# Optimization experiments

Measured on AMD Instinct MI355X. Metric: run time of the kernel, lower is better.

Reference implementation:

```python
import jax, jax.numpy as jnp
import numpy as np

B, C, H8, W8 = 2, 256, 56, 96
RADIUS, LEVELS = 4, 4


def setup_inputs() -> dict:
    key = jax.random.key(0)
    k1, k2, k3, k4, k5 = jax.random.split(key, 5)
    fmap1 = jax.random.normal(k1, (B, C, H8, W8), jnp.float32)
    fmap2 = jax.random.normal(k2, (B, C, H8, W8), jnp.float32)
    xs = jnp.arange(W8, dtype=jnp.float32)
    ys = jnp.arange(H8, dtype=jnp.float32)
    bx, by = jnp.broadcast_arrays(xs[None, :], ys[:, None])
    base = jnp.stack([bx, by], axis=0)  # [2,H8,W8], x first (as create_coords_grid)
    coords = base[None] + 4.0 * jax.random.normal(k3, (B, 2, H8, W8), jnp.float32)
    flow = jax.random.normal(k4, (B, 2, H8, W8), jnp.float32)
    mask = jax.random.normal(k5, (B, 9 * 8 * 8, H8, W8), jnp.float32)
    return {"fmap1": fmap1, "fmap2": fmap2, "coords": coords, "flow": flow, "mask": mask}


def _bilinear_sample(cflat, Hl, Wl, px, py):
    # cflat: [N, Hl*Wl]; px,py: [N,P] pixel coords; zero padding outside (grid_sample default)
    x0 = jnp.floor(px)
    y0 = jnp.floor(py)
    wx = px - x0
    wy = py - y0
    x0 = x0.astype(jnp.int32)
    y0 = y0.astype(jnp.int32)

    def g(xi, yi):
        valid = (xi >= 0) & (xi <= Wl - 1) & (yi >= 0) & (yi <= Hl - 1)
        idx = jnp.clip(yi, 0, Hl - 1) * Wl + jnp.clip(xi, 0, Wl - 1)
        return jnp.where(valid, jnp.take_along_axis(cflat, idx, axis=1), 0.0)

    return ((1 - wy) * ((1 - wx) * g(x0, y0) + wx * g(x0 + 1, y0))
            + wy * ((1 - wx) * g(x0, y0 + 1) + wx * g(x0 + 1, y0 + 1)))


def _corr_lookup(fmap1, fmap2, coords):
    b, c, h, w = fmap1.shape
    n = b * h * w
    # all-pairs correlation, scaled by sqrt(C)
    corr = jnp.einsum('bchw,bcij->bhwij', fmap1, fmap2) / jnp.sqrt(jnp.float32(c))
    cl = corr.reshape(n, h, w)
    # query coords (pixel units at level 0)
    cx = coords[:, 0].reshape(n)
    cy = coords[:, 1].reshape(n)
    r = RADIUS
    lin = jnp.linspace(-r, r, 2 * r + 1, dtype=jnp.float32)
    # replicates torch.meshgrid(dy,dx) quirk: x-offset varies along axis 0, y along axis 1
    xo = jnp.repeat(lin, 2 * r + 1)  # [81]
    yo = jnp.tile(lin, 2 * r + 1)    # [81]
    outs = []
    for i in range(LEVELS):
        Hl, Wl = cl.shape[1], cl.shape[2]
        cflat = cl.reshape(n, Hl * Wl)
        px = cx[:, None] / (2 ** i) + xo[None, :]
        py = cy[:, None] / (2 ** i) + yo[None, :]
        samp = _bilinear_sample(cflat, Hl, Wl, px, py)  # [N,81]
        outs.append(samp.reshape(b, h, w, -1))
        if i < LEVELS - 1:  # 2x2 avg pool, stride 2
            cl = cl.reshape(n, Hl // 2, 2, Wl // 2, 2).mean(axis=(2, 4))
    out = jnp.concatenate(outs, axis=-1)  # [B,h,w,4*81]
    return out.transpose(0, 3, 1, 2)


def _convex_upsample(flow, mask):
    b, ch, h, w = flow.shape
    m = mask.reshape(b, 1, 9, 8, 8, h, w)
    m = jax.nn.softmax(m, axis=2)
    fp = jnp.pad(8.0 * flow, ((0, 0), (0, 0), (1, 1), (1, 1)))
    # 3x3 unfold, kernel positions row-major (matches F.unfold ordering)
    patches = jnp.stack([fp[:, :, i:i + h, j:j + w]
                         for i in range(3) for j in range(3)], axis=2)  # [B,2,9,h,w]
    up = jnp.sum(m * patches[:, :, :, None, None], axis=2)  # [B,2,8,8,h,w]
    up = up.transpose(0, 1, 4, 2, 5, 3)  # [B,2,h,8,w,8]
    return up.reshape(b, ch, 8 * h, 8 * w)


def reference(fmap1, fmap2, coords, flow, mask):
    corr_feats = _corr_lookup(fmap1, fmap2, coords)  # [B,324,H8,W8]
    up_flow = _convex_upsample(flow, mask)           # [B,2,8*H8,8*W8]
    return (corr_feats, up_flow)
```

## Files before the change

### kernel.cpp

```cpp
#include <hip/hip_runtime.h>
#include <math.h>

constexpr int B = 2, C = 256, H = 56, W = 96;
constexpr int HW = H * W;
constexpr int RADIUS = 4;

#define SQ 21.166666f
constexpr float SCL = 36.0f / (127.0f * 127.0f * 16.0f);

constexpr size_t F1T_B = 0;
constexpr size_t L0_B  = (size_t)B * HW * C;
constexpr size_t L1_B  = L0_B + (size_t)B * HW * C;
constexpr size_t L2_B  = L1_B + (size_t)B * 28 * 48 * C;
constexpr size_t L3_B  = L2_B + (size_t)B * 14 * 24 * C;
constexpr size_t OUT0_ELEMS = (size_t)B * 324 * HW;

static __device__ __forceinline__ int dot4acc(int a, int b, int c) {
#if __has_builtin(__builtin_amdgcn_sdot4)
    return __builtin_amdgcn_sdot4(a, b, c, false);
#else
    c += (int)(char)(a) * (int)(char)(b);
    c += (int)(char)(a >> 8) * (int)(char)(b >> 8);
    c += (int)(char)(a >> 16) * (int)(char)(b >> 16);
    c += (int)(char)(a >> 24) * (int)(char)(b >> 24);
    return c;
#endif
}

static __device__ __forceinline__ unsigned short pack_i8x2(float a, float b) {
    int ia = (int)rintf(a); ia = ia < -127 ? -127 : (ia > 127 ? 127 : ia);
    int ib = (int)rintf(b); ib = ib < -127 ? -127 : (ib > 127 ? 127 : ib);
    return (unsigned short)((ia & 0xFF) | ((ib & 0xFF) << 8));
}

constexpr int TP_BLOCKS = (HW / 32) * (C / 64) * 2 * B;
constexpr int CU_BLOCKS = B * H * 8;
__global__ __launch_bounds__(256) void prep_kernel(
    const float* __restrict__ fmap1, const float* __restrict__ fmap2,
    const float* __restrict__ flow, const float* __restrict__ mask,
    char* __restrict__ ws, float* __restrict__ out1) {
    __shared__ float smem[72 * 96 + 2 * 3 * 98];
    int bid = blockIdx.x;
    int tid = threadIdx.x;

    if (bid < TP_BLOCKS) {
        float (*tile)[33] = (float(*)[33])smem;
        int zi = bid / 672;
        int rem = bid % 672;
        int by = rem / 168, bx = rem % 168;
        int b = zi & 1, m = zi >> 1;
        const float* src = m ? fmap2 : fmap1;
        unsigned short* dst = (unsigned short*)(ws + (m ? L0_B : F1T_B));
        int c0 = by * 64, q0 = bx * 32;
        int tx = tid & 31, ty = tid >> 5;
#pragma unroll
        for (int r = 0; r < 8; ++r) {
            int cl = ty + r * 8;
            tile[cl][tx] = src[((size_t)(b * C + c0 + cl)) * HW + q0 + tx];
        }
        __syncthreads();
#pragma unroll
        for (int r = 0; r < 4; ++r) {
            int pl = ty + r * 8;
            dst[((size_t)b * HW + q0 + pl) * 128 + (c0 >> 1) + tx] =
                pack_i8x2(tile[2 * tx][pl] * SQ, tile[2 * tx + 1][pl] * SQ);
        }
        return;
    }

    float* msk = smem;
    float* fst = smem + 72 * 96;
    int cb = bid - TP_BLOCKS;
    int i = cb & 7;
    int r = cb >> 3;
    int h = r % H;
    int b = r / H;

    for (int idx = tid; idx < 72 * 96; idx += 256) {
        int row = idx / 96, wc = idx - row * 96;
        int k = row >> 3, j = row & 7;
        int gl = k * 64 + i * 8 + j;
        msk[idx] = mask[((size_t)(b * 576 + gl)) * HW + h * W + wc];
    }
    for (int idx = tid; idx < 588; idx += 256) {
        int ch = idx / 294;
        int rem2 = idx - ch * 294;
        int rr = rem2 / 98;
        int xw = rem2 - rr * 98;
        int hh = h + rr - 1, ww = xw - 1;
        float v = 0.f;
        if (hh >= 0 && hh < H && ww >= 0 && ww < W)
            v = 8.0f * flow[((size_t)(b * 2 + ch)) * HW + hh * W + ww];
        fst[idx] = v;
    }
    __syncthreads();

#pragma unroll
    for (int rr = 0; rr < 3; ++rr) {
        int col = tid + rr * 256;
        int w = col >> 3, j = col & 7;
        float m[9], mx = -1e30f;
#pragma unroll
        for (int k = 0; k < 9; ++k) {
            m[k] = msk[(k * 8 + j) * 96 + w];
            mx = fmaxf(mx, m[k]);
        }
        float sum = 0.f;
#pragma unroll
        for (int k = 0; k < 9; ++k) {
            m[k] = __expf(m[k] - mx);
            sum += m[k];
        }
        float inv = 1.0f / sum;
        float a0 = 0.f, a1 = 0.f;
#pragma unroll
        for (int k = 0; k < 9; ++k) {
            int ki = k / 3, kj = k - ki * 3;
            float wgt = m[k] * inv;
            a0 = fmaf(wgt, fst[0 * 294 + ki * 98 + w + kj], a0);
            a1 = fmaf(wgt, fst[1 * 294 + ki * 98 + w + kj], a1);
        }
        size_t row8 = (size_t)8 * h + i;
        out1[((size_t)(b * 2 + 0) * 448 + row8) * 768 + col] = a0;
        out1[((size_t)(b * 2 + 1) * 448 + row8) * 768 + col] = a1;
    }
}

constexpr int NP1 = B * 28 * 48 * C / 2;
constexpr int NP2 = B * 14 * 24 * C / 2;
constexpr int NP3 = B * 7 * 12 * C / 2;

template <int S>
static __device__ __forceinline__ void pool_accum(const unsigned short* src,
                                                  int& sx, int& sy) {
#pragma unroll
    for (int dy = 0; dy < S; ++dy)
#pragma unroll
        for (int dx = 0; dx < S; ++dx) {
            unsigned short v = src[(size_t)dy * (W * 128) + dx * 128];
            sx += (int)(char)(v & 0xFF);
            sy += (int)(char)(v >> 8);
        }
}

__global__ __launch_bounds__(256) void build_pools(char* __restrict__ ws) {
    const unsigned short* L0p = (const unsigned short*)(ws + L0_B);
    int t = blockIdx.x * 256 + threadIdx.x;
    int l, tl;
    if (t < NP1)             { l = 1; tl = t; }
    else if (t < NP1 + NP2)  { l = 2; tl = t - NP1; }
    else                     { l = 3; tl = t - NP1 - NP2; }
    int Wo = W >> l, Ho = H >> l, S = 1 << l;
    int c2 = tl & 127;
    int r = tl >> 7;
    int x = r % Wo; r /= Wo;
    int y = r % Ho;
    int b = r / Ho;
    const unsigned short* src =
        L0p + ((size_t)(b * H + y * S) * W + x * S) * 128 + c2;
    int sx = 0, sy = 0;
    if (l == 1)      pool_accum<2>(src, sx, sy);
    else if (l == 2) pool_accum<4>(src, sx, sy);
    else             pool_accum<8>(src, sx, sy);
    float inv = 1.0f / (S * S);
    unsigned short* dst = (unsigned short*)(ws + (l == 1 ? L1_B : (l == 2 ? L2_B : L3_B)));
    dst[tl] = pack_i8x2((float)sx * inv, (float)sy * inv);
}

__global__ __launch_bounds__(256, 8) void corr_fused(
    const float* __restrict__ coords, const char* __restrict__ ws,
    float* __restrict__ out0) {
    __shared__ float Dsh[4][4][101];
    __shared__ float Wxy[4][4][2];

    int tid = threadIdx.x;
    int l = tid >> 6;
    int lane = tid & 63;
    int v = lane & 3;
    int grp = lane >> 2;

    int g0 = blockIdx.x * 4;
    int b = g0 / HW;
    int hw0 = g0 - b * HW;

    int Hl = H >> l, Wl = W >> l;
    size_t off = (l == 0 ? L0_B : (l == 1 ? L1_B : (l == 2 ? L2_B : L3_B)));
    const char* base8 = ws + off + (size_t)b * Hl * Wl * C;
    float scale = (l == 0 ? 1.0f : (l == 1 ? 0.5f : (l == 2 ? 0.25f : 0.125f)));

    int xo0 = grp < 10 ? grp : grp - 10;
    int yo0 = grp < 10 ? 0 : 1;

    const char* f1b = ws + F1T_B;

#pragma unroll 1
    for (int qi = 0; qi < 4; ++qi) {
        int g = g0 + qi;
        const char* ab = f1b + (size_t)g * C + (v << 4);
        int4 A0 = *(const int4*)(ab);
        int4 A1 = *(const int4*)(ab + 64);
        int4 A2 = *(const int4*)(ab + 128);
        int4 A3 = *(const int4*)(ab + 192);

        float cx = coords[(size_t)(b * 2 + 0) * HW + hw0 + qi];
        float cy = coords[(size_t)(b * 2 + 1) * HW + hw0 + qi];
        float fx = cx * scale, fy = cy * scale;
        float fxf = floorf(fx), fyf = floorf(fy);
        float wx = fx - fxf, wy = fy - fyf;
        int ix = (int)fxf, iy = (int)fyf;
        if (lane == 0) { Wxy[l][qi][0] = wx; Wxy[l][qi][1] = wy; }

        int xo = xo0, yo = yo0;
#pragma unroll
        for (int it = 0; it < 7; ++it) {
            bool live = (it < 6) | (grp < 4);
            int x = ix - RADIUS + xo;
            int y = iy - RADIUS + yo;
            int s0 = 0, s1 = 0, s2 = 0, s3 = 0;
            if (live && (unsigned)x < (unsigned)Wl && (unsigned)y < (unsigned)Hl) {
                const char* rp = base8 + (((size_t)(y * Wl + x)) << 8) + (v << 4);
                int4 c0 = *(const int4*)(rp);
                int4 c1 = *(const int4*)(rp + 64);
                int4 c2 = *(const int4*)(rp + 128);
                int4 c3 = *(const int4*)(rp + 192);
                s0 = dot4acc(c0.x, A0.x, s0); s1 = dot4acc(c0.y, A0.y, s1);
                s2 = dot4acc(c0.z, A0.z, s2); s3 = dot4acc(c0.w, A0.w, s3);
                s0 = dot4acc(c1.x, A1.x, s0); s1 = dot4acc(c1.y, A1.y, s1);
                s2 = dot4acc(c1.z, A1.z, s2); s3 = dot4acc(c1.w, A1.w, s3);
                s0 = dot4acc(c2.x, A2.x, s0); s1 = dot4acc(c2.y, A2.y, s1);
                s2 = dot4acc(c2.z, A2.z, s2); s3 = dot4acc(c2.w, A2.w, s3);
                s0 = dot4acc(c3.x, A3.x, s0); s1 = dot4acc(c3.y, A3.y, s1);
                s2 = dot4acc(c3.z, A3.z, s2); s3 = dot4acc(c3.w, A3.w, s3);
            }
            int s = (s0 + s1) + (s2 + s3);
            s += __shfl_xor(s, 1);
            s += __shfl_xor(s, 2);
            if (v == 0 && live) Dsh[l][qi][it * 16 + grp] = (float)s * SCL;
            xo += 6;
            int cr = xo >= 10;
            xo -= cr ? 10 : 0;
            yo += 1 + cr;
        }
    }
    __syncthreads();

    for (int o = tid; o < 324 * 4; o += 256) {
        int q = o & 3, ch = o >> 2;
        int lv = ch / 81;
        int o81 = ch - lv * 81;
        int xo = o81 / 9;
        int yo = o81 - xo * 9;
        float wxv = Wxy[lv][q][0], wyv = Wxy[lv][q][1];
        const float* D = Dsh[lv][q];
        float v00 = D[yo * 10 + xo];
        float v01 = D[yo * 10 + xo + 1];
        float v10 = D[yo * 10 + xo + 10];
        float v11 = D[yo * 10 + xo + 11];
        float res = (1.f - wyv) * ((1.f - wxv) * v00 + wxv * v01)
                  +        wyv  * ((1.f - wxv) * v10 + wxv * v11);
        out0[((size_t)(b * 324 + ch)) * HW + hw0 + q] = res;
    }
}

extern "C" void kernel_launch(void* const* d_in, const int* in_sizes, int n_in,
                              void* d_out, int out_size, void* d_ws, size_t ws_size,
                              hipStream_t stream) {
    const float* fmap1  = (const float*)d_in[0];
    const float* fmap2  = (const float*)d_in[1];
    const float* coords = (const float*)d_in[2];
    const float* flow   = (const float*)d_in[3];
    const float* maskp  = (const float*)d_in[4];
    float* out = (float*)d_out;
    char* ws = (char*)d_ws;

    prep_kernel<<<TP_BLOCKS + CU_BLOCKS, 256, 0, stream>>>(
        fmap1, fmap2, flow, maskp, ws, out + OUT0_ELEMS);
    build_pools<<<(NP1 + NP2 + NP3) / 256, 256, 0, stream>>>(ws);
    corr_fused<<<B * HW / 4, 256, 0, stream>>>(coords, ws, out);
}
```

Before: 155.0 us.

## Map each corr block to one pyramid level over 16 queries, branchless gathers

Reorganizes corr_fused so each block handles one pyramid level for 16 query pixels (4 waves x 4 queries), instead of all four levels for 4 queries. Same-level gathers within a block now hit nearby rows, and output stores write 16 contiguous pixels per channel instead of 4, improving coalescing. The bounds-checked branch is replaced by clamped unconditional loads with the result masked afterward, which removes divergence but adds loads for out-of-range and dead lanes. Launch bounds drop to 6 blocks per CU.

```diff
diff --git a/kernel.cpp b/kernel.cpp
--- a/kernel.cpp
+++ b/kernel.cpp
@@ -167,23 +167,28 @@
     dst[tl] = pack_i8x2((float)sx * inv, (float)sy * inv);
 }
 
-__global__ __launch_bounds__(256, 8) void corr_fused(
+constexpr int QB = 672;
+__global__ __launch_bounds__(256, 6) void corr_fused(
     const float* __restrict__ coords, const char* __restrict__ ws,
     float* __restrict__ out0) {
-    __shared__ float Dsh[4][4][101];
-    __shared__ float Wxy[4][4][2];
+    __shared__ float Dsh[16][101];
+    __shared__ float Wxy[16][2];
 
     int tid = threadIdx.x;
-    int l = tid >> 6;
+    int wave = tid >> 6;
     int lane = tid & 63;
     int v = lane & 3;
     int grp = lane >> 2;
 
-    int g0 = blockIdx.x * 4;
+    int bid = blockIdx.x;
+    int l = bid / QB;
+    int qb = bid - l * QB;
+    int g0 = qb * 16;
     int b = g0 / HW;
     int hw0 = g0 - b * HW;
 
     int Hl = H >> l, Wl = W >> l;
+    int Wlm1 = Wl - 1, Hlm1 = Hl - 1;
     size_t off = (l == 0 ? L0_B : (l == 1 ? L1_B : (l == 2 ? L2_B : L3_B)));
     const char* base8 = ws + off + (size_t)b * Hl * Wl * C;
     float scale = (l == 0 ? 1.0f : (l == 1 ? 0.5f : (l == 2 ? 0.25f : 0.125f)));
@@ -195,47 +200,50 @@
 
 #pragma unroll 1
     for (int qi = 0; qi < 4; ++qi) {
-        int g = g0 + qi;
+        int wq = wave * 4 + qi;
+        int g = g0 + wq;
         const char* ab = f1b + (size_t)g * C + (v << 4);
         int4 A0 = *(const int4*)(ab);
         int4 A1 = *(const int4*)(ab + 64);
         int4 A2 = *(const int4*)(ab + 128);
         int4 A3 = *(const int4*)(ab + 192);
 
-        float cx = coords[(size_t)(b * 2 + 0) * HW + hw0 + qi];
-        float cy = coords[(size_t)(b * 2 + 1) * HW + hw0 + qi];
+        float cx = coords[(size_t)(b * 2 + 0) * HW + hw0 + wq];
+        float cy = coords[(size_t)(b * 2 + 1) * HW + hw0 + wq];
         float fx = cx * scale, fy = cy * scale;
         float fxf = floorf(fx), fyf = floorf(fy);
         float wx = fx - fxf, wy = fy - fyf;
         int ix = (int)fxf, iy = (int)fyf;
-        if (lane == 0) { Wxy[l][qi][0] = wx; Wxy[l][qi][1] = wy; }
+        if (lane == 0) { Wxy[wq][0] = wx; Wxy[wq][1] = wy; }
 
         int xo = xo0, yo = yo0;
 #pragma unroll
         for (int it = 0; it < 7; ++it) {
-            bool live = (it < 6) | (grp < 4);
             int x = ix - RADIUS + xo;
             int y = iy - RADIUS + yo;
+            bool valid = ((unsigned)x < (unsigned)Wl) & ((unsigned)y < (unsigned)Hl);
+            int xc = min(max(x, 0), Wlm1);
+            int yc = min(max(y, 0), Hlm1);
+            const char* rp = base8 + ((yc * Wl + xc) << 8) + (v << 4);
+            int4 c0 = *(const int4*)(rp);
+            int4 c1 = *(const int4*)(rp + 64);
+            int4 c2 = *(const int4*)(rp + 128);
+            int4 c3 = *(const int4*)(rp + 192);
             int s0 = 0, s1 = 0, s2 = 0, s3 = 0;
-            if (live && (unsigned)x < (unsigned)Wl && (unsigned)y < (unsigned)Hl) {
-                const char* rp = base8 + (((size_t)(y * Wl + x)) << 8) + (v << 4);
-                int4 c0 = *(const int4*)(rp);
-                int4 c1 = *(const int4*)(rp + 64);
-                int4 c2 = *(const int4*)(rp + 128);
-                int4 c3 = *(const int4*)(rp + 192);
-                s0 = dot4acc(c0.x, A0.x, s0); s1 = dot4acc(c0.y, A0.y, s1);
-                s2 = dot4acc(c0.z, A0.z, s2); s3 = dot4acc(c0.w, A0.w, s3);
-                s0 = dot4acc(c1.x, A1.x, s0); s1 = dot4acc(c1.y, A1.y, s1);
-                s2 = dot4acc(c1.z, A1.z, s2); s3 = dot4acc(c1.w, A1.w, s3);
-                s0 = dot4acc(c2.x, A2.x, s0); s1 = dot4acc(c2.y, A2.y, s1);
-                s2 = dot4acc(c2.z, A2.z, s2); s3 = dot4acc(c2.w, A2.w, s3);
-                s0 = dot4acc(c3.x, A3.x, s0); s1 = dot4acc(c3.y, A3.y, s1);
-                s2 = dot4acc(c3.z, A3.z, s2); s3 = dot4acc(c3.w, A3.w, s3);
-            }
+            s0 = dot4acc(c0.x, A0.x, s0); s1 = dot4acc(c0.y, A0.y, s1);
+            s2 = dot4acc(c0.z, A0.z, s2); s3 = dot4acc(c0.w, A0.w, s3);
+            s0 = dot4acc(c1.x, A1.x, s0); s1 = dot4acc(c1.y, A1.y, s1);
+            s2 = dot4acc(c1.z, A1.z, s2); s3 = dot4acc(c1.w, A1.w, s3);
+            s0 = dot4acc(c2.x, A2.x, s0); s1 = dot4acc(c2.y, A2.y, s1);
+            s2 = dot4acc(c2.z, A2.z, s2); s3 = dot4acc(c2.w, A2.w, s3);
+            s0 = dot4acc(c3.x, A3.x, s0); s1 = dot4acc(c3.y, A3.y, s1);
+            s2 = dot4acc(c3.z, A3.z, s2); s3 = dot4acc(c3.w, A3.w, s3);
             int s = (s0 + s1) + (s2 + s3);
+            s = valid ? s : 0;
             s += __shfl_xor(s, 1);
             s += __shfl_xor(s, 2);
-            if (v == 0 && live) Dsh[l][qi][it * 16 + grp] = (float)s * SCL;
+            bool live = (it < 6) | (grp < 4);
+            if (v == 0 && live) Dsh[wq][it * 16 + grp] = (float)s * SCL;
             xo += 6;
             int cr = xo >= 10;
             xo -= cr ? 10 : 0;
@@ -244,21 +252,20 @@
     }
     __syncthreads();
 
-    for (int o = tid; o < 324 * 4; o += 256) {
-        int q = o & 3, ch = o >> 2;
-        int lv = ch / 81;
-        int o81 = ch - lv * 81;
-        int xo = o81 / 9;
-        int yo = o81 - xo * 9;
-        float wxv = Wxy[lv][q][0], wyv = Wxy[lv][q][1];
-        const float* D = Dsh[lv][q];
+    int chbase = l * 81;
+    for (int o = tid; o < 81 * 16; o += 256) {
+        int q = o & 15, ch = o >> 4;
+        int xo = ch / 9;
+        int yo = ch - xo * 9;
+        float wxv = Wxy[q][0], wyv = Wxy[q][1];
+        const float* D = Dsh[q];
         float v00 = D[yo * 10 + xo];
         float v01 = D[yo * 10 + xo + 1];
         float v10 = D[yo * 10 + xo + 10];
         float v11 = D[yo * 10 + xo + 11];
         float res = (1.f - wyv) * ((1.f - wxv) * v00 + wxv * v01)
                   +        wyv  * ((1.f - wxv) * v10 + wxv * v11);
-        out0[((size_t)(b * 324 + ch)) * HW + hw0 + q] = res;
+        out0[((size_t)(b * 324 + chbase + ch)) * HW + hw0 + q] = res;
     }
 }
 
@@ -276,5 +283,5 @@
     prep_kernel<<<TP_BLOCKS + CU_BLOCKS, 256, 0, stream>>>(
         fmap1, fmap2, flow, maskp, ws, out + OUT0_ELEMS);
     build_pools<<<(NP1 + NP2 + NP3) / 256, 256, 0, stream>>>(ws);
-    corr_fused<<<B * HW / 4, 256, 0, stream>>>(coords, ws, out);
-}
+    corr_fused<<<4 * QB, 256, 0, stream>>>(coords, ws, out);
+}
```

After: 152.2 us. No clear change (-1.8%).
